# Optimization experiments

Measured on AMD Instinct MI355X. Metric: run time of the kernel, lower is better.

The kernel has to match this reference:

```python
import jax, jax.numpy as jnp
import numpy as np
import math

B, S, D, H = 2, 2048, 4096, 32
HD = D // H  # 128


def setup_inputs() -> dict:
    key = jax.random.key(0)
    ks = jax.random.split(key, 8)
    x = jax.random.normal(ks[0], (B, S, D), dtype=jnp.float32)
    wq = jax.random.normal(ks[1], (D, D), dtype=jnp.float32) * 0.02
    wk = jax.random.normal(ks[2], (D, D), dtype=jnp.float32) * 0.02
    wv = jax.random.normal(ks[3], (D, D), dtype=jnp.float32) * 0.02
    wo = jax.random.normal(ks[4], (D, D), dtype=jnp.float32) * 0.02
    # RoPE frequencies as in LLaMA: theta = 10000^{-2i/hd}
    inv_freq = 1.0 / (10000.0 ** (np.arange(0, HD, 2, dtype=np.float32) / HD))  # [HD/2]
    t = np.arange(S, dtype=np.float32)
    freqs = np.outer(t, inv_freq)  # [S, HD/2]
    freqs_cos = jnp.asarray(np.cos(freqs))
    freqs_sin = jnp.asarray(np.sin(freqs))
    # additive causal mask [1,1,S,S]
    neg = jnp.full((S, S), -1e9, dtype=jnp.float32)
    mask = jnp.triu(neg, k=1)[None, None, :, :]
    return {"x": x, "wq": wq, "wk": wk, "wv": wv, "wo": wo,
            "freqs_cos": freqs_cos, "freqs_sin": freqs_sin, "mask": mask}


def _apply_rope(t, cos, sin):
    # t: [b, s, h, hd]; cos/sin: [s, hd/2]. Complex mult on (even, odd) pairs.
    tr = t.reshape(*t.shape[:-1], HD // 2, 2)
    xr, xi = tr[..., 0], tr[..., 1]
    c = cos[None, :, None, :]
    s = sin[None, :, None, :]
    out_r = xr * c - xi * s
    out_i = xr * s + xi * c
    return jnp.stack([out_r, out_i], axis=-1).reshape(t.shape)


def reference(x, wq, wk, wv, wo, freqs_cos, freqs_sin, mask):
    b, s, d = x.shape
    # projections (nn.Linear: y = x @ W^T)
    xq = (x @ wq.T).reshape(b, s, H, HD)
    xk = (x @ wk.T).reshape(b, s, H, HD)
    xv = (x @ wv.T).reshape(b, s, H, HD)
    xq = _apply_rope(xq, freqs_cos, freqs_sin)
    xk = _apply_rope(xk, freqs_cos, freqs_sin)
    # [b,h,q,k] scores, softmax in fp32, then attend
    scores = jnp.einsum('bqhd,bkhd->bhqk', xq, xk) / math.sqrt(HD)
    scores = scores + mask
    probs = jax.nn.softmax(scores.astype(jnp.float32), axis=-1).astype(xq.dtype)
    out = jnp.einsum('bhqk,bkhd->bqhd', probs, xv).reshape(b, s, d)
    return out @ wo.T
```

## Files before the change

### kernel.cpp

```cpp
#include <hip/hip_runtime.h>

typedef __bf16 bf16x8 __attribute__((ext_vector_type(8)));
typedef float f32x4 __attribute__((ext_vector_type(4)));
typedef float f32x16 __attribute__((ext_vector_type(16)));
typedef unsigned short u16;
typedef unsigned int u32;
typedef u16 u16x8 __attribute__((ext_vector_type(8)));
typedef u16 u16x4 __attribute__((ext_vector_type(4)));
typedef u32 u32x4 __attribute__((ext_vector_type(4)));

#define B_ 2
#define S_ 2048
#define D_ 4096
#define H_ 32
#define HD_ 128
#define SM_SCALE 0.08838834764831845f
#define C2_ 0.12751743f

__device__ __forceinline__ u16 f2bf(float f) {
  __bf16 h = (__bf16)f;
  return __builtin_bit_cast(unsigned short, h);
}
__device__ __forceinline__ float bf2f(u16 u) {
  return (float)__builtin_bit_cast(__bf16, u);
}

#define GLD_TO_LDS16(gsrc, ldst)                                                     \
  __builtin_amdgcn_global_load_lds((__attribute__((address_space(1))) void*)(gsrc),  \
                                   (__attribute__((address_space(3))) void*)(ldst),  \
                                   16, 0, 0)

__global__ __launch_bounds__(256) void cvt5_kernel(const float* __restrict__ s0,
                                                   const float* __restrict__ s1,
                                                   const float* __restrict__ s2,
                                                   const float* __restrict__ s3,
                                                   const float* __restrict__ s4,
                                                   u16* __restrict__ d0,
                                                   u16* __restrict__ d1,
                                                   u16* __restrict__ d2,
                                                   u16* __restrict__ d3,
                                                   u16* __restrict__ d4,
                                                   int n4) {
  const int region = blockIdx.x >> 9;
  const float* src = region == 0 ? s0 : region == 1 ? s1 : region == 2 ? s2
                   : region == 3 ? s3 : s4;
  u16* dst = region == 0 ? d0 : region == 1 ? d1 : region == 2 ? d2
           : region == 3 ? d3 : d4;
  int i = (blockIdx.x & 511) * 256 + threadIdx.x;
  const int stride = 512 * 256;
  for (; i < n4; i += stride) {
    float4 v = reinterpret_cast<const float4*>(src)[i];
    u16x4 o;
    o[0] = f2bf(v.x); o[1] = f2bf(v.y); o[2] = f2bf(v.z); o[3] = f2bf(v.w);
    reinterpret_cast<u16x4*>(dst)[i] = o;
  }
}


#define LGKM0()                                            \
  do {                                                     \
    asm volatile("s_waitcnt lgkmcnt(0)" ::: "memory");     \
    __builtin_amdgcn_sched_barrier(0);                     \
  } while (0)

__device__ __forceinline__ void fill_af(bf16x8 (&dst)[4], const u16* half_base,
                                        int wr, int lane, int ks) {
#pragma unroll
  for (int m = 0; m < 4; ++m) {
    int rr = wr * 64 + m * 16 + (lane & 15);
    int c8 = (ks * 4 + (lane >> 4)) ^ (rr & 7);
    dst[m] = *reinterpret_cast<const bf16x8*>(half_base + rr * 64 + c8 * 8);
  }
}
__device__ __forceinline__ void fill_bf(bf16x8 (&dst)[2][2], const u16* half_base,
                                        int wn, int lane) {
#pragma unroll
  for (int ks = 0; ks < 2; ++ks)
#pragma unroll
    for (int n = 0; n < 2; ++n) {
      int rr = wn * 32 + n * 16 + (lane & 15);
      int c8 = (ks * 4 + (lane >> 4)) ^ (rr & 7);
      dst[ks][n] = *reinterpret_cast<const bf16x8*>(half_base + rr * 64 + c8 * 8);
    }
}

#define MFMA8(MQ, NQ, KS, AF, BF)                                                \
  do {                                                                           \
    __builtin_amdgcn_s_setprio(1);                                               \
    _Pragma("unroll") for (int m = 0; m < 4; ++m)                                \
      _Pragma("unroll") for (int n = 0; n < 2; ++n)                              \
        acc[(MQ) * 4 + m][(NQ) * 2 + n] =                                        \
            __builtin_amdgcn_mfma_f32_16x16x32_bf16(                             \
                (AF)[m], (BF)[KS][n], acc[(MQ) * 4 + m][(NQ) * 2 + n], 0, 0, 0); \
    __builtin_amdgcn_s_setprio(0);                                               \
  } while (0)

template <typename OutT, bool ROPE>
__global__ __launch_bounds__(512, 2) void gemm256_kernel(const u16* __restrict__ A,
                                                         const u16* __restrict__ Bw,
                                                         OutT* __restrict__ C,
                                                         int M, int N, int K,
                                                         const float* __restrict__ fc,
                                                         const float* __restrict__ fs) {
  __shared__ u16 As[2][2][8192];
  __shared__ u16 Bs[2][2][8192];
  const int tid = threadIdx.x;
  const int lane = tid & 63;
  const int w = tid >> 6;
  const int wr = w >> 2;
  const int wn = w & 3;
  const int nbx = N >> 8;
  const int nby = M >> 8;
  const int nwg = nby * nbx;
  int tr, tc;
  if (nby == 16 && nbx == 16) {
    int xcd = blockIdx.x & 7, j = blockIdx.x >> 3;
    tr = (xcd >> 1) * 4 + (j >> 3);
    tc = (xcd & 1) * 8 + (j & 7);
  } else {
    int wg = blockIdx.x;
    if ((nwg & 7) == 0) wg = (wg & 7) * (nwg >> 3) + (wg >> 3);
    tr = wg / nbx; tc = wg % nbx;
  }

  const size_t arow0 = (size_t)tr * 256;
  const size_t brow0 = (size_t)tc * 256;
  const int KT = K >> 6;

  auto stageA = [&](int t, int half) {
    if (t >= KT) return;
    const int k0 = t << 6;
    u16* base = &As[t & 1][half][0];
#pragma unroll
    for (int i = 0; i < 2; ++i) {
      int q = i * 512 + tid;
      int r = q >> 3;
      int c8 = (q & 7) ^ (r & 7);
      GLD_TO_LDS16(A + (arow0 + half * 128 + r) * K + k0 + c8 * 8, base + q * 8);
    }
  };
  auto stageB = [&](int t, int half) {
    if (t >= KT) return;
    const int k0 = t << 6;
    u16* base = &Bs[t & 1][half][0];
#pragma unroll
    for (int i = 0; i < 2; ++i) {
      int q = i * 512 + tid;
      int r = q >> 3;
      int c8 = (q & 7) ^ (r & 7);
      GLD_TO_LDS16(Bw + (brow0 + half * 128 + r) * K + k0 + c8 * 8, base + q * 8);
    }
  };

  f32x4 acc[8][4] = {};
  bf16x8 afX[4], afY[4], bf0[2][2], bf1[2][2];

  stageA(0, 0); stageA(0, 1); stageB(0, 0); stageB(0, 1);
  stageB(1, 0); stageB(1, 1); stageA(1, 1);
  asm volatile("s_waitcnt vmcnt(4)" ::: "memory");
  __builtin_amdgcn_s_barrier();
  __builtin_amdgcn_sched_barrier(0);
  fill_af(afX, &As[0][0][0], wr, lane, 0);
  fill_bf(bf0, &Bs[0][0][0], wn, lane);

  for (int k = 0; k < KT; ++k) {
    const int buf = k & 1, nb = buf ^ 1;
    const u16* A0 = &As[buf][0][0];
    const u16* A1 = &As[buf][1][0];
    const u16* B1L = &Bs[buf][1][0];
    const u16* A0n = &As[nb][0][0];
    const u16* B0n = &Bs[nb][0][0];

    LGKM0();
    fill_af(afY, A0, wr, lane, 1);
    fill_bf(bf1, B1L, wn, lane);
    stageA(k + 1, 0);
    MFMA8(0, 0, 0, afX, bf0);
    LGKM0();
    fill_af(afX, A1, wr, lane, 0);
    MFMA8(0, 0, 1, afY, bf0);
    __builtin_amdgcn_s_barrier();

    LGKM0();
    fill_af(afY, A1, wr, lane, 1);
    stageB(k + 2, 0);
    MFMA8(1, 0, 0, afX, bf0);
    LGKM0();
    fill_af(afX, A1, wr, lane, 0);
    MFMA8(1, 0, 1, afY, bf0);
    __builtin_amdgcn_s_barrier();

    LGKM0();
    fill_af(afY, A1, wr, lane, 1);
    stageB(k + 2, 1);
    MFMA8(1, 1, 0, afX, bf1);
    LGKM0();
    fill_af(afX, A0, wr, lane, 0);
    MFMA8(1, 1, 1, afY, bf1);
    __builtin_amdgcn_s_barrier();

    LGKM0();
    fill_af(afY, A0, wr, lane, 1);
    MFMA8(0, 1, 0, afX, bf1);
    LGKM0();
    stageA(k + 2, 1);
    if (k >= KT - 3) asm volatile("s_waitcnt vmcnt(0)" ::: "memory");
    else             asm volatile("s_waitcnt vmcnt(4)" ::: "memory");
    __builtin_amdgcn_s_barrier();
    __builtin_amdgcn_sched_barrier(0);
    if (k + 1 < KT) {
      fill_af(afX, A0n, wr, lane, 0);
      fill_bf(bf0, B0n, wn, lane);
    }
    MFMA8(0, 1, 1, afY, bf1);
    __builtin_amdgcn_s_barrier();
  }

#pragma unroll
  for (int mi = 0; mi < 8; ++mi) {
    const int mq = mi >> 2, m = mi & 3;
#pragma unroll
    for (int ni = 0; ni < 4; ++ni) {
      const int nq = ni >> 1, n = ni & 1;
#pragma unroll
      for (int r = 0; r < 4; ++r) {
        size_t row = arow0 + mq * 128 + wr * 64 + m * 16 + ((lane >> 4) << 2) + r;
        size_t col = (size_t)tc * 256 + nq * 128 + wn * 32 + n * 16 + (lane & 15);
        float v = acc[mi][ni][r];
        if constexpr (ROPE) {
          float o = __shfl_xor(v, 1);
          int s = (int)(row & (S_ - 1));
          int p = (wn * 32 + n * 16 + (lane & 14)) >> 1;
          float cv = fc[(s << 6) + p];
          float sv = fs[(s << 6) + p];
          v = (lane & 1) ? (v * cv + o * sv) : (v * cv - o * sv);
        }
        if constexpr (__is_same(OutT, float)) {
          C[row * N + col] = v;
        } else {
          C[row * N + col] = f2bf(v);
        }
      }
    }
  }
}

__global__ __launch_bounds__(512, 2) void attn_kernel(const u16* __restrict__ Q,
                                                      const u16* __restrict__ K,
                                                      const u16* __restrict__ V,
                                                      u16* __restrict__ O) {
  __shared__ u16 Ks[2][64 * 128];
  __shared__ u16 Vt[2][128 * 64];

  const int blk = blockIdx.x;
  const int qt = 7 - (blk >> 6);
  const int bh = blk & 63;
  const int b = bh >> 5, h = bh & 31;
  const int q0 = qt << 8;
  const int tid = threadIdx.x, lane = tid & 63, w = tid >> 6;
  const int wq0 = q0 + w * 32;
  const int l31 = lane & 31;
  const int hi = lane >> 5;
  const int qg = wq0 + l31;

  const int r0 = lane >> 1;
  const int dc = 2 * w + (lane & 1);
  const int vd0 = dc * 8;

  bf16x8 qf[8];
#pragma unroll
  for (int kb = 0; kb < 8; ++kb)
    qf[kb] = *reinterpret_cast<const bf16x8*>(Q + (size_t)(b * S_ + qg) * D_ + h * HD_ + kb * 16 + hi * 8);

  f32x16 oacc[4] = {};
  float mrun = -__builtin_inff(), lrun = 0.f;

  const int ntiles = 4 * qt + 4;
  u16x8 vr0, vr1;

  {
#pragma unroll
    for (int it = 0; it < 2; ++it) {
      int ff = it * 512 + tid;
      int row = ff >> 4, cc = ff & 15;
      int scc = cc ^ (row & 7);
      GLD_TO_LDS16(K + (size_t)(b * S_ + row) * D_ + h * HD_ + scc * 8, &Ks[0][ff << 3]);
    }
    vr0 = *reinterpret_cast<const u16x8*>(V + (size_t)(b * S_ + 2 * r0) * D_ + h * HD_ + vd0);
    vr1 = *reinterpret_cast<const u16x8*>(V + (size_t)(b * S_ + 2 * r0 + 1) * D_ + h * HD_ + vd0);
    u32* vt32 = reinterpret_cast<u32*>(&Vt[0][0]);
#pragma unroll
    for (int j = 0; j < 8; ++j) {
      int d = vd0 + j;
      u32 val = (u32)vr0[j] | ((u32)vr1[j] << 16);
      vt32[d * 32 + ((r0 >> 2) ^ j) * 4 + (r0 & 3)] = val;
    }
  }
  __syncthreads();

  for (int t = 0; t < ntiles; ++t) {
    const int cur = t & 1, nxt = cur ^ 1;
    const bool pre = (t + 1 < ntiles);
    if (pre) {
      const int kv1 = (t + 1) << 6;
#pragma unroll
      for (int it = 0; it < 2; ++it) {
        int ff = it * 512 + tid;
        int row = ff >> 4, cc = ff & 15;
        int scc = cc ^ (row & 7);
        GLD_TO_LDS16(K + (size_t)(b * S_ + kv1 + row) * D_ + h * HD_ + scc * 8, &Ks[nxt][ff << 3]);
      }
      vr0 = *reinterpret_cast<const u16x8*>(V + (size_t)(b * S_ + kv1 + 2 * r0) * D_ + h * HD_ + vd0);
      vr1 = *reinterpret_cast<const u16x8*>(V + (size_t)(b * S_ + kv1 + 2 * r0 + 1) * D_ + h * HD_ + vd0);
    }

    const int kv0 = t << 6;
    if (kv0 <= wq0 + 31) {
      f32x16 st[2] = {};
      __builtin_amdgcn_s_setprio(1);
#pragma unroll
      for (int kvh = 0; kvh < 2; ++kvh) {
#pragma unroll
        for (int kb = 0; kb < 8; ++kb) {
          int row = kvh * 32 + l31;
          int cc = (2 * kb + hi) ^ (row & 7);
          bf16x8 kf = *reinterpret_cast<const bf16x8*>(&Ks[cur][(row << 7) + (cc << 3)]);
          st[kvh] = __builtin_amdgcn_mfma_f32_32x32x16_bf16(kf, qf[kb], st[kvh], 0, 0, 0);
        }
      }
      __builtin_amdgcn_s_setprio(0);

      if (kv0 + 63 > wq0) {
#pragma unroll
        for (int kvh = 0; kvh < 2; ++kvh)
#pragma unroll
          for (int r = 0; r < 16; ++r) {
            int kvg = kv0 + kvh * 32 + (r & 3) + 8 * (r >> 2) + 4 * hi;
            if (kvg > qg) st[kvh][r] = -1e30f;
          }
      }

      float vmax = -1e30f;
#pragma unroll
      for (int kvh = 0; kvh < 2; ++kvh)
#pragma unroll
        for (int r = 0; r < 16; ++r) vmax = fmaxf(vmax, st[kvh][r]);
      vmax = fmaxf(vmax, __shfl_xor(vmax, 32));
      if (!__all(vmax <= mrun + 64.0f)) {
        float mnew = fmaxf(mrun, vmax);
        float sc = exp2f((mrun - mnew) * C2_);
        mrun = mnew;
        lrun *= sc;
#pragma unroll
        for (int db = 0; db < 4; ++db)
#pragma unroll
          for (int r = 0; r < 16; ++r) oacc[db][r] *= sc;
      }
      float psum = 0.f;
#pragma unroll
      for (int kvh = 0; kvh < 2; ++kvh)
#pragma unroll
        for (int r = 0; r < 16; ++r) {
          float p = exp2f((st[kvh][r] - mrun) * C2_);
          st[kvh][r] = p;
          psum += p;
        }
      psum += __shfl_xor(psum, 32);
      lrun += psum;

      __builtin_amdgcn_s_setprio(1);
#pragma unroll
      for (int h2 = 0; h2 < 2; ++h2)
#pragma unroll
        for (int s2 = 0; s2 < 2; ++s2) {
          const int rb = s2 * 8;
          u32 w0, w1, w2, w3;
          asm("v_cvt_pk_bf16_f32 %0, %1, %2" : "=v"(w0) : "v"(st[h2][rb + 0]), "v"(st[h2][rb + 1]));
          asm("v_cvt_pk_bf16_f32 %0, %1, %2" : "=v"(w1) : "v"(st[h2][rb + 2]), "v"(st[h2][rb + 3]));
          asm("v_cvt_pk_bf16_f32 %0, %1, %2" : "=v"(w2) : "v"(st[h2][rb + 4]), "v"(st[h2][rb + 5]));
          asm("v_cvt_pk_bf16_f32 %0, %1, %2" : "=v"(w3) : "v"(st[h2][rb + 6]), "v"(st[h2][rb + 7]));
          u32 sw0 = (u32)__shfl_xor((int)w0, 32);
          u32 sw1 = (u32)__shfl_xor((int)w1, 32);
          u32 sw2 = (u32)__shfl_xor((int)w2, 32);
          u32 sw3 = (u32)__shfl_xor((int)w3, 32);
          u32x4 fw;
          fw[0] = hi ? sw2 : w0;
          fw[1] = hi ? sw3 : w1;
          fw[2] = hi ? w2 : sw0;
          fw[3] = hi ? w3 : sw1;
          bf16x8 pfrag = __builtin_bit_cast(bf16x8, fw);
#pragma unroll
          for (int db = 0; db < 4; ++db) {
            int d = db * 32 + l31;
            int cc = (h2 * 4 + s2 * 2 + hi) ^ (d & 7);
            bf16x8 va = *reinterpret_cast<const bf16x8*>(&Vt[cur][(d << 6) + (cc << 3)]);
            oacc[db] = __builtin_amdgcn_mfma_f32_32x32x16_bf16(va, pfrag, oacc[db], 0, 0, 0);
          }
        }
      __builtin_amdgcn_s_setprio(0);
    }

    if (pre) {
      u32* vt32 = reinterpret_cast<u32*>(&Vt[nxt][0]);
#pragma unroll
      for (int j = 0; j < 8; ++j) {
        int d = vd0 + j;
        u32 val = (u32)vr0[j] | ((u32)vr1[j] << 16);
        vt32[d * 32 + ((r0 >> 2) ^ j) * 4 + (r0 & 3)] = val;
      }
    }
    __syncthreads();
  }

  const float rinv = 1.0f / lrun;
#pragma unroll
  for (int db = 0; db < 4; ++db)
#pragma unroll
    for (int g = 0; g < 4; ++g) {
      u16x4 o4;
#pragma unroll
      for (int j = 0; j < 4; ++j) o4[j] = f2bf(oacc[db][g * 4 + j] * rinv);
      int d = db * 32 + g * 8 + 4 * hi;
      *reinterpret_cast<u16x4*>(O + (size_t)(b * S_ + qg) * D_ + h * HD_ + d) = o4;
    }
}

extern "C" void kernel_launch(void* const* d_in, const int* in_sizes, int n_in,
                              void* d_out, int out_size, void* d_ws, size_t ws_size,
                              hipStream_t stream) {
  const float* x = (const float*)d_in[0];
  const float* wq = (const float*)d_in[1];
  const float* wk = (const float*)d_in[2];
  const float* wv = (const float*)d_in[3];
  const float* wo = (const float*)d_in[4];
  const float* fc = (const float*)d_in[5];
  const float* fs = (const float*)d_in[6];
  float* out = (float*)d_out;

  const size_t SLOT = (size_t)B_ * S_ * D_;
  u16* ws = (u16*)d_ws;
  u16* wqb = ws + 0 * SLOT;
  u16* wkb = ws + 1 * SLOT;
  u16* wvb = ws + 2 * SLOT;
  u16* wob = ws + 3 * SLOT;
  u16* xb  = ws + 4 * SLOT;
  u16* Qb  = ws + 5 * SLOT;
  u16* Kb  = ws + 6 * SLOT;
  u16* Vb  = ws + 7 * SLOT;
  u16* Ob  = xb;

  const int n4 = (int)(SLOT / 4);
  cvt5_kernel<<<2560, 256, 0, stream>>>(x, wq, wk, wv, wo, xb, wqb, wkb, wvb, wob, n4);

  gemm256_kernel<u16, true><<<256, 512, 0, stream>>>(xb, wqb, Qb, B_ * S_, D_, D_, fc, fs);
  gemm256_kernel<u16, true><<<256, 512, 0, stream>>>(xb, wkb, Kb, B_ * S_, D_, D_, fc, fs);
  gemm256_kernel<u16, false><<<256, 512, 0, stream>>>(xb, wvb, Vb, B_ * S_, D_, D_, fc, fs);

  attn_kernel<<<512, 512, 0, stream>>>(Qb, Kb, Vb, Ob);

  gemm256_kernel<float, false><<<256, 512, 0, stream>>>(Ob, wob, out, B_ * S_, D_, D_, fc, fs);
}
```

Before: 680.2 us.

## Defer PV MFMA by one tile to overlap softmax with matrix math

```diff
diff --git a/kernel.cpp b/kernel.cpp
--- a/kernel.cpp
+++ b/kernel.cpp
@@ -250,7 +250,7 @@
                                                       const u16* __restrict__ V,
                                                       u16* __restrict__ O) {
   __shared__ u16 Ks[2][64 * 128];
-  __shared__ u16 Vt[2][128 * 64];
+  __shared__ u16 Vt[3][128 * 64];
 
   const int blk = blockIdx.x;
   const int qt = 7 - (blk >> 6);
@@ -277,6 +277,9 @@
 
   const int ntiles = 4 * qt + 4;
   u16x8 vr0, vr1;
+  bf16x8 pf[4];
+  bool have_pf = false;
+  int pvbuf = 0;
 
   {
 #pragma unroll
@@ -315,8 +318,10 @@
     }
 
     const int kv0 = t << 6;
-    if (kv0 <= wq0 + 31) {
-      f32x16 st[2] = {};
+    const bool active = (kv0 <= wq0 + 31);
+    f32x16 st[2] = {};
+
+    if (active) {
       __builtin_amdgcn_s_setprio(1);
 #pragma unroll
       for (int kvh = 0; kvh < 2; ++kvh) {
@@ -329,7 +334,26 @@
         }
       }
       __builtin_amdgcn_s_setprio(0);
-
+    }
+
+    if (have_pf) {
+      const u16* vb = &Vt[pvbuf][0];
+      __builtin_amdgcn_s_setprio(1);
+#pragma unroll
+      for (int pi = 0; pi < 4; ++pi) {
+#pragma unroll
+        for (int db = 0; db < 4; ++db) {
+          int d = db * 32 + l31;
+          int cc = (pi * 2 + hi) ^ (d & 7);
+          bf16x8 va = *reinterpret_cast<const bf16x8*>(vb + (d << 6) + (cc << 3));
+          oacc[db] = __builtin_amdgcn_mfma_f32_32x32x16_bf16(va, pf[pi], oacc[db], 0, 0, 0);
+        }
+      }
+      __builtin_amdgcn_s_setprio(0);
+      have_pf = false;
+    }
+
+    if (active) {
       if (kv0 + 63 > wq0) {
 #pragma unroll
         for (int kvh = 0; kvh < 2; ++kvh)
@@ -339,7 +363,6 @@
             if (kvg > qg) st[kvh][r] = -1e30f;
           }
       }
-
       float vmax = -1e30f;
 #pragma unroll
       for (int kvh = 0; kvh < 2; ++kvh)
@@ -368,7 +391,6 @@
       psum += __shfl_xor(psum, 32);
       lrun += psum;
 
-      __builtin_amdgcn_s_setprio(1);
 #pragma unroll
       for (int h2 = 0; h2 < 2; ++h2)
 #pragma unroll
@@ -388,20 +410,14 @@
           fw[1] = hi ? sw3 : w1;
           fw[2] = hi ? w2 : sw0;
           fw[3] = hi ? w3 : sw1;
-          bf16x8 pfrag = __builtin_bit_cast(bf16x8, fw);
-#pragma unroll
-          for (int db = 0; db < 4; ++db) {
-            int d = db * 32 + l31;
-            int cc = (h2 * 4 + s2 * 2 + hi) ^ (d & 7);
-            bf16x8 va = *reinterpret_cast<const bf16x8*>(&Vt[cur][(d << 6) + (cc << 3)]);
-            oacc[db] = __builtin_amdgcn_mfma_f32_32x32x16_bf16(va, pfrag, oacc[db], 0, 0, 0);
-          }
-        }
-      __builtin_amdgcn_s_setprio(0);
+          pf[h2 * 2 + s2] = __builtin_bit_cast(bf16x8, fw);
+        }
+      pvbuf = t % 3;
+      have_pf = true;
     }
 
     if (pre) {
-      u32* vt32 = reinterpret_cast<u32*>(&Vt[nxt][0]);
+      u32* vt32 = reinterpret_cast<u32*>(&Vt[(t + 1) % 3][0]);
 #pragma unroll
       for (int j = 0; j < 8; ++j) {
         int d = vd0 + j;
@@ -410,6 +426,20 @@
       }
     }
     __syncthreads();
+  }
+
+  if (have_pf) {
+    const u16* vb = &Vt[pvbuf][0];
+#pragma unroll
+    for (int pi = 0; pi < 4; ++pi) {
+#pragma unroll
+      for (int db = 0; db < 4; ++db) {
+        int d = db * 32 + l31;
+        int cc = (pi * 2 + hi) ^ (d & 7);
+        bf16x8 va = *reinterpret_cast<const bf16x8*>(vb + (d << 6) + (cc << 3));
+        oacc[db] = __builtin_amdgcn_mfma_f32_32x32x16_bf16(va, pf[pi], oacc[db], 0, 0, 0);
+      }
+    }
   }
 
   const float rinv = 1.0f / lrun;
```

After: 686.9 us. No clear change (+1.0%).
